# Performance work log

Hardware: AMD Instinct MI355X
Metric: run time of the kernel (lower is better)

The kernel has to match this reference:

```python
import jax, jax.numpy as jnp
import numpy as np

B, T, D, S = 32, 4096, 512, 256
SCALE = 0.1  # time_bias_scale


def setup_inputs() -> dict:
    key = jax.random.key(0)
    ks = jax.random.split(key, 9)
    return {
        "context": jax.random.normal(ks[0], (B, T, D), jnp.float32),
        "t_star": jax.random.uniform(ks[1], (B,), jnp.float32),
        "t_context": jax.random.uniform(ks[2], (B, T, 1), jnp.float32),
        "W1": jax.random.normal(ks[3], (1, D), jnp.float32) / np.sqrt(1.0),
        "b1": jax.random.normal(ks[4], (D,), jnp.float32) * 0.02,
        "W2": jax.random.normal(ks[5], (D, D), jnp.float32) / np.sqrt(D),
        "b2": jax.random.normal(ks[6], (D,), jnp.float32) * 0.02,
        "Wout": jax.random.normal(ks[7], (D, 2 * S), jnp.float32) / np.sqrt(D),
        "bout": jax.random.normal(ks[8], (2 * S,), jnp.float32) * 0.02,
    }


def reference(context, t_star, t_context, W1, b1, W2, b2, Wout, bout):
    # query embed: Linear(1,D) -> SiLU -> Linear(D,D)
    h = jax.nn.silu(t_star[:, None] @ W1 + b1)        # (B, D)
    q = h @ W2 + b2                                   # (B, D)
    # single-query attention scores with additive time bias
    scores = jnp.einsum('bd,btd->bt', q, context)     # (B, T)
    time_bias = -jnp.abs(t_star[:, None] - t_context[..., 0]) / SCALE  # (B, T)
    weights = jax.nn.softmax(scores + time_bias, axis=-1)
    pooled = jnp.einsum('bt,btd->bd', weights, context)  # (B, D)
    out = pooled @ Wout + bout                            # (B, 2S)
    mu, log_sigma = out[:, :S], out[:, S:]
    return (mu, log_sigma)
```

## Files before the change

### kernel.cpp

```cpp
#include <hip/hip_runtime.h>
#include <math.h>

#define BB 32
#define TT 4096
#define DD 512
#define SS 256
#define SEG 128
#define GRP 16
static constexpr float INV_SCALE = 10.0f;

__global__ __launch_bounds__(512) void k_q(
    const float* __restrict__ t_star, const float* __restrict__ W1,
    const float* __restrict__ b1, const float* __restrict__ W2,
    const float* __restrict__ b2, float* __restrict__ q) {
  const int b   = blockIdx.x >> 3;
  const int jg  = blockIdx.x & 7;
  const int tid = threadIdx.x;
  const int di  = tid & 63;
  const int kg  = tid >> 6;
  __shared__ float h[DD];
  __shared__ float red[8][64];
  {
    float x = t_star[b] * W1[tid] + b1[tid];
    h[tid] = x / (1.0f + __expf(-x));
  }
  __syncthreads();
  const float* w = W2 + jg * 64 + di;
  float acc = 0.0f;
#pragma unroll 8
  for (int kk = 0; kk < 64; ++kk) {
    const int k = kg * 64 + kk;
    acc += h[k] * w[(size_t)k * DD];
  }
  red[kg][di] = acc;
  __syncthreads();
  if (tid < 64) {
    float s = 0.0f;
#pragma unroll
    for (int g = 0; g < 8; ++g) s += red[g][tid];
    q[b * DD + jg * 64 + tid] = s + b2[jg * 64 + tid];
  }
}

#define GLDS(gp, lp)                                                        \
  __builtin_amdgcn_global_load_lds(                                         \
      (const __attribute__((address_space(1))) void*)(gp),                  \
      (__attribute__((address_space(3))) void*)(lp), 16, 0, 2 )

__global__ __launch_bounds__(256) void k_fused(
    const float* __restrict__ ctx, const float* __restrict__ q,
    const float* __restrict__ t_star, const float* __restrict__ t_ctx,
    float* __restrict__ part_pool,
    float* __restrict__ part_ms) {
  __shared__ __align__(16) float lds[4][3][2 * DD];
  const int wid  = threadIdx.x >> 6;
  const int lane = threadIdx.x & 63;
  const int w    = blockIdx.x * 4 + wid;
  const int b    = w >> 7;
  const int s    = w & 127;

  const float4* qp = (const float4*)(q + b * DD);
  const float4 q0 = qp[lane];
  const float4 q1 = qp[64 + lane];
  const float ts = t_star[b];
  const float2 tc = *(const float2*)(t_ctx + b * TT + ((lane & 15) * 2 * SEG + 2 * s));
  const float tbx = -fabsf(ts - tc.x) * INV_SCALE;
  const float tby = -fabsf(ts - tc.y) * INV_SCALE;

  float m = -INFINITY, l = 0.0f;
  float4 p0 = {0, 0, 0, 0}, p1 = {0, 0, 0, 0};

  const float* cb = ctx + ((size_t)b * TT + 2 * s) * DD;

#pragma unroll
  for (int g = 0; g < 2; ++g) {
    const float* gb = cb + (size_t)g * 2 * SEG * DD;
    float* sb = &lds[wid][g][0];
#pragma unroll
    for (int piece = 0; piece < 4; ++piece)
      GLDS(gb + piece * 256 + lane * 4, sb + piece * 256);
  }

#pragma unroll
  for (int g = 0; g < GRP; ++g) {
    if (g + 2 < GRP) {
      const float* gb = cb + (size_t)(g + 2) * 2 * SEG * DD;
      float* sb = &lds[wid][(g + 2) % 3][0];
#pragma unroll
      for (int piece = 0; piece < 4; ++piece)
        GLDS(gb + piece * 256 + lane * 4, sb + piece * 256);
      asm volatile("s_waitcnt vmcnt(8)" ::: "memory");
    } else if (g + 2 == GRP) {
      asm volatile("s_waitcnt vmcnt(4)" ::: "memory");
    } else {
      asm volatile("s_waitcnt vmcnt(0)" ::: "memory");
    }

    const float4* sf = (const float4*)&lds[wid][g % 3][0];
    const float4 x0 = sf[lane];
    const float4 x1 = sf[64 + lane];
    const float4 y0 = sf[128 + lane];
    const float4 y1 = sf[192 + lane];

    float s0 = x0.x * q0.x + x0.y * q0.y + x0.z * q0.z + x0.w * q0.w +
               x1.x * q1.x + x1.y * q1.y + x1.z * q1.z + x1.w * q1.w;
    float s1 = y0.x * q0.x + y0.y * q0.y + y0.z * q0.z + y0.w * q0.w +
               y1.x * q1.x + y1.y * q1.y + y1.z * q1.z + y1.w * q1.w;
#pragma unroll
    for (int off = 32; off > 0; off >>= 1) {
      s0 += __shfl_xor(s0, off);
      s1 += __shfl_xor(s1, off);
    }
    s0 += __shfl(tbx, g);
    s1 += __shfl(tby, g);

    const float gm = fmaxf(s0, s1);
    const float nm = fmaxf(m, gm);
    const float sc = __expf(m - nm);
    m = nm;
    const float e0 = __expf(s0 - m);
    const float e1 = __expf(s1 - m);
    l = l * sc + e0 + e1;
    p0.x = p0.x * sc + e0 * x0.x + e1 * y0.x;
    p0.y = p0.y * sc + e0 * x0.y + e1 * y0.y;
    p0.z = p0.z * sc + e0 * x0.z + e1 * y0.z;
    p0.w = p0.w * sc + e0 * x0.w + e1 * y0.w;
    p1.x = p1.x * sc + e0 * x1.x + e1 * y1.x;
    p1.y = p1.y * sc + e0 * x1.y + e1 * y1.y;
    p1.z = p1.z * sc + e0 * x1.z + e1 * y1.z;
    p1.w = p1.w * sc + e0 * x1.w + e1 * y1.w;
  }

  float4* pp = (float4*)(part_pool + (size_t)w * DD);
  pp[lane] = p0;
  pp[64 + lane] = p1;
  if (lane == 0) {
    part_ms[w * 2 + 0] = m;
    part_ms[w * 2 + 1] = l;
  }
}

__global__ __launch_bounds__(512) void k_merge(
    const float* __restrict__ part_pool, const float* __restrict__ part_ms,
    float* __restrict__ pool) {
  const int b   = blockIdx.x >> 2;
  const int dg  = blockIdx.x & 3;
  const int tid = threadIdx.x;
  const int lane = tid & 63;
  const int base = b * SEG;
  __shared__ float scl[SEG];
  __shared__ float red[4][128];

  const float mA = part_ms[(base + lane) * 2 + 0];
  const float mB = part_ms[(base + 64 + lane) * 2 + 0];
  const float lA = part_ms[(base + lane) * 2 + 1];
  const float lB = part_ms[(base + 64 + lane) * 2 + 1];
  float M = fmaxf(mA, mB);
#pragma unroll
  for (int off = 32; off > 0; off >>= 1) M = fmaxf(M, __shfl_xor(M, off));
  float Z = __expf(mA - M) * lA + __expf(mB - M) * lB;
#pragma unroll
  for (int off = 32; off > 0; off >>= 1) Z += __shfl_xor(Z, off);
  const float invZ = 1.0f / Z;
  if (tid < SEG) scl[tid] = __expf(part_ms[(base + tid) * 2] - M);
  __syncthreads();

  const int dl = tid & 127;
  const int cg = tid >> 7;
  float acc = 0.0f;
#pragma unroll 8
  for (int i = 0; i < 32; ++i) {
    const int c = cg * 32 + i;
    acc += scl[c] * part_pool[((size_t)base + c) * DD + dg * 128 + dl];
  }
  red[cg][dl] = acc;
  __syncthreads();
  if (tid < 128)
    pool[b * DD + dg * 128 + tid] =
        (red[0][tid] + red[1][tid] + red[2][tid] + red[3][tid]) * invZ;
}

__global__ __launch_bounds__(256) void k_out(
    const float* __restrict__ pool, const float* __restrict__ Wout,
    const float* __restrict__ bout, float* __restrict__ out) {
  const int b   = blockIdx.x >> 3;
  const int jg  = blockIdx.x & 7;
  const int tid = threadIdx.x;
  const int kg  = tid >> 6;
  const int j   = tid & 63;
  const int jc  = jg * 64 + j;
  __shared__ float p[DD];
  __shared__ float red[4][64];

  p[tid] = pool[b * DD + tid];
  p[tid + 256] = pool[b * DD + 256 + tid];
  __syncthreads();

  float acc = 0.0f;
#pragma unroll 8
  for (int kk = 0; kk < 128; ++kk) {
    const int k = kg * 128 + kk;
    acc += p[k] * Wout[(size_t)k * DD + jc];
  }
  red[kg][j] = acc;
  __syncthreads();
  if (tid < 64) {
    const int jj = jg * 64 + tid;
    float o = red[0][tid] + red[1][tid] + red[2][tid] + red[3][tid] + bout[jj];
    if (jj < SS) out[b * SS + jj] = o;
    else         out[BB * SS + b * SS + (jj - SS)] = o;
  }
}

extern "C" void kernel_launch(void* const* d_in, const int* in_sizes, int n_in,
                              void* d_out, int out_size, void* d_ws, size_t ws_size,
                              hipStream_t stream) {
  const float* ctx    = (const float*)d_in[0];
  const float* t_star = (const float*)d_in[1];
  const float* t_ctx  = (const float*)d_in[2];
  const float* W1     = (const float*)d_in[3];
  const float* b1     = (const float*)d_in[4];
  const float* W2     = (const float*)d_in[5];
  const float* b2     = (const float*)d_in[6];
  const float* Wout   = (const float*)d_in[7];
  const float* bout   = (const float*)d_in[8];
  float* out = (float*)d_out;

  float* ws = (float*)d_ws;
  float* q         = ws;
  float* part_pool = q + (size_t)BB * DD;
  float* part_ms   = part_pool + (size_t)BB * SEG * DD;
  float* pool      = part_ms + (size_t)BB * SEG * 2;

  k_q<<<BB * 8, 512, 0, stream>>>(t_star, W1, b1, W2, b2, q);
  k_fused<<<BB * SEG / 4, 256, 0, stream>>>(ctx, q, t_star, t_ctx, part_pool, part_ms);
  k_merge<<<BB * 4, 512, 0, stream>>>(part_pool, part_ms, pool);
  k_out<<<BB * 8, 256, 0, stream>>>(pool, Wout, bout, out);
}
```

Baseline: 66.45 us.

## Repartition fused attention into 96 interleaved segments per batch across 768 blocks

Changes the work split so each batch has 96 wave-segments instead of 128. Each wave walks row pairs interleaved with stride 96 and handles 21 or 22 groups, giving 768 blocks, which is meant to match the CU count and avoid a partial tail wave. The merge kernel is adjusted for 96 partials with masked lanes, and the partial stores become nontemporal. The trade-off is that the group loop now has a runtime trip count with rotating slot indices and is no longer fully unrolled, and the per-wave work is uneven (21 vs 22 groups).

```diff
diff --git a/kernel.cpp b/kernel.cpp
--- a/kernel.cpp
+++ b/kernel.cpp
@@ -5,9 +5,11 @@
 #define TT 4096
 #define DD 512
 #define SS 256
-#define SEG 128
-#define GRP 16
+#define WPB 96
+#define NBLK 768
 static constexpr float INV_SCALE = 10.0f;
+
+typedef float f32x4 __attribute__((ext_vector_type(4)));
 
 __global__ __launch_bounds__(512) void k_q(
     const float* __restrict__ t_star, const float* __restrict__ W1,
@@ -55,48 +57,53 @@
   __shared__ __align__(16) float lds[4][3][2 * DD];
   const int wid  = threadIdx.x >> 6;
   const int lane = threadIdx.x & 63;
-  const int w    = blockIdx.x * 4 + wid;
-  const int b    = w >> 7;
-  const int s    = w & 127;
+  const int W    = blockIdx.x * 4 + wid;
+  const int b    = W / WPB;
+  const int v    = W % WPB;
+  const int NG   = (v < 32) ? 22 : 21;
 
   const float4* qp = (const float4*)(q + b * DD);
   const float4 q0 = qp[lane];
   const float4 q1 = qp[64 + lane];
   const float ts = t_star[b];
-  const float2 tc = *(const float2*)(t_ctx + b * TT + ((lane & 15) * 2 * SEG + 2 * s));
+
+  const int lg = lane & 31;
+  int gidx = lg * WPB + v;
+  if (gidx >= TT / 2) gidx = v;
+  const float2 tc = *(const float2*)(t_ctx + b * TT + 2 * gidx);
   const float tbx = -fabsf(ts - tc.x) * INV_SCALE;
   const float tby = -fabsf(ts - tc.y) * INV_SCALE;
 
   float m = -INFINITY, l = 0.0f;
   float4 p0 = {0, 0, 0, 0}, p1 = {0, 0, 0, 0};
 
-  const float* cb = ctx + ((size_t)b * TT + 2 * s) * DD;
+  const float* cbatch = ctx + (size_t)b * TT * DD;
 
 #pragma unroll
   for (int g = 0; g < 2; ++g) {
-    const float* gb = cb + (size_t)g * 2 * SEG * DD;
+    const float* gb = cbatch + (size_t)(g * WPB + v) * 2 * DD;
     float* sb = &lds[wid][g][0];
 #pragma unroll
     for (int piece = 0; piece < 4; ++piece)
       GLDS(gb + piece * 256 + lane * 4, sb + piece * 256);
   }
 
-#pragma unroll
-  for (int g = 0; g < GRP; ++g) {
-    if (g + 2 < GRP) {
-      const float* gb = cb + (size_t)(g + 2) * 2 * SEG * DD;
-      float* sb = &lds[wid][(g + 2) % 3][0];
+  int rs = 0, wslot = 2;
+  for (int g = 0; g < NG; ++g) {
+    if (g + 2 < NG) {
+      const float* gb = cbatch + (size_t)((g + 2) * WPB + v) * 2 * DD;
+      float* sb = &lds[wid][wslot][0];
 #pragma unroll
       for (int piece = 0; piece < 4; ++piece)
         GLDS(gb + piece * 256 + lane * 4, sb + piece * 256);
       asm volatile("s_waitcnt vmcnt(8)" ::: "memory");
-    } else if (g + 2 == GRP) {
+    } else if (g + 2 == NG) {
       asm volatile("s_waitcnt vmcnt(4)" ::: "memory");
     } else {
       asm volatile("s_waitcnt vmcnt(0)" ::: "memory");
     }
 
-    const float4* sf = (const float4*)&lds[wid][g % 3][0];
+    const float4* sf = (const float4*)&lds[wid][rs][0];
     const float4 x0 = sf[lane];
     const float4 x1 = sf[64 + lane];
     const float4 y0 = sf[128 + lane];
@@ -129,14 +136,19 @@
     p1.y = p1.y * sc + e0 * x1.y + e1 * y1.y;
     p1.z = p1.z * sc + e0 * x1.z + e1 * y1.z;
     p1.w = p1.w * sc + e0 * x1.w + e1 * y1.w;
-  }
-
-  float4* pp = (float4*)(part_pool + (size_t)w * DD);
-  pp[lane] = p0;
-  pp[64 + lane] = p1;
+
+    rs = (rs == 2) ? 0 : rs + 1;
+    wslot = (wslot == 2) ? 0 : wslot + 1;
+  }
+
+  f32x4* pp = (f32x4*)(part_pool + (size_t)W * DD);
+  f32x4 v0 = {p0.x, p0.y, p0.z, p0.w};
+  f32x4 v1 = {p1.x, p1.y, p1.z, p1.w};
+  __builtin_nontemporal_store(v0, pp + lane);
+  __builtin_nontemporal_store(v1, pp + 64 + lane);
   if (lane == 0) {
-    part_ms[w * 2 + 0] = m;
-    part_ms[w * 2 + 1] = l;
+    part_ms[W * 2 + 0] = m;
+    part_ms[W * 2 + 1] = l;
   }
 }
 
@@ -147,30 +159,33 @@
   const int dg  = blockIdx.x & 3;
   const int tid = threadIdx.x;
   const int lane = tid & 63;
-  const int base = b * SEG;
-  __shared__ float scl[SEG];
+  const int base = b * WPB;
+  __shared__ float scl[WPB];
   __shared__ float red[4][128];
 
   const float mA = part_ms[(base + lane) * 2 + 0];
-  const float mB = part_ms[(base + 64 + lane) * 2 + 0];
   const float lA = part_ms[(base + lane) * 2 + 1];
-  const float lB = part_ms[(base + 64 + lane) * 2 + 1];
+  float mB = -INFINITY, lB = 0.0f;
+  if (lane < WPB - 64) {
+    mB = part_ms[(base + 64 + lane) * 2 + 0];
+    lB = part_ms[(base + 64 + lane) * 2 + 1];
+  }
   float M = fmaxf(mA, mB);
 #pragma unroll
   for (int off = 32; off > 0; off >>= 1) M = fmaxf(M, __shfl_xor(M, off));
-  float Z = __expf(mA - M) * lA + __expf(mB - M) * lB;
+  float Z = __expf(mA - M) * lA + ((lane < WPB - 64) ? __expf(mB - M) * lB : 0.0f);
 #pragma unroll
   for (int off = 32; off > 0; off >>= 1) Z += __shfl_xor(Z, off);
   const float invZ = 1.0f / Z;
-  if (tid < SEG) scl[tid] = __expf(part_ms[(base + tid) * 2] - M);
+  if (tid < WPB) scl[tid] = __expf(part_ms[(base + tid) * 2] - M);
   __syncthreads();
 
   const int dl = tid & 127;
   const int cg = tid >> 7;
   float acc = 0.0f;
 #pragma unroll 8
-  for (int i = 0; i < 32; ++i) {
-    const int c = cg * 32 + i;
+  for (int i = 0; i < 24; ++i) {
+    const int c = cg * 24 + i;
     acc += scl[c] * part_pool[((size_t)base + c) * DD + dg * 128 + dl];
   }
   red[cg][dl] = acc;
@@ -229,11 +244,11 @@
   float* ws = (float*)d_ws;
   float* q         = ws;
   float* part_pool = q + (size_t)BB * DD;
-  float* part_ms   = part_pool + (size_t)BB * SEG * DD;
-  float* pool      = part_ms + (size_t)BB * SEG * 2;
+  float* part_ms   = part_pool + (size_t)BB * WPB * DD;
+  float* pool      = part_ms + (size_t)BB * WPB * 2;
 
   k_q<<<BB * 8, 512, 0, stream>>>(t_star, W1, b1, W2, b2, q);
-  k_fused<<<BB * SEG / 4, 256, 0, stream>>>(ctx, q, t_star, t_ctx, part_pool, part_ms);
+  k_fused<<<NBLK, 256, 0, stream>>>(ctx, q, t_star, t_ctx, part_pool, part_ms);
   k_merge<<<BB * 4, 512, 0, stream>>>(part_pool, part_ms, pool);
   k_out<<<BB * 8, 256, 0, stream>>>(pool, Wout, bout, out);
 }
```

Measured after the change: 61.61 us, median of 2. 7.3% less time.
